# Performance work log

Hardware: AMD Instinct MI355X
Metric: run time of the kernel (lower is better)

## Reference

```python
import jax, jax.numpy as jnp
import numpy as np

SEQ, B, I, H, L = 2048, 32, 1024, 1024, 2


def setup_inputs() -> dict:
    key = jax.random.key(0)
    ks = jax.random.split(key, 6)
    k = 1.0 / np.sqrt(H)
    x = jax.random.normal(ks[0], (SEQ, B, I), dtype=jnp.float32)
    h0 = jnp.zeros((L, B, H), dtype=jnp.float32)
    # layer 0 W_ih is [H, I]; with I == H all layers stack to [L, H, H]
    W_ih = jax.random.uniform(ks[1], (L, H, H), minval=-k, maxval=k, dtype=jnp.float32)
    W_hh = jax.random.uniform(ks[2], (L, H, H), minval=-k, maxval=k, dtype=jnp.float32)
    b_ih = jax.random.uniform(ks[3], (L, H), minval=-k, maxval=k, dtype=jnp.float32)
    b_hh = jax.random.uniform(ks[4], (L, H), minval=-k, maxval=k, dtype=jnp.float32)
    return {"x": x, "h0": h0, "W_ih": W_ih, "W_hh": W_hh, "b_ih": b_ih, "b_hh": b_hh}


def reference(x, h0, W_ih, W_hh, b_ih, b_hh):
    """Stacked tanh RNN, seq-first input [T, B, I]. Returns (h_history [T,B,H], h_T [L,B,H])."""
    num_layers = W_ih.shape[0]

    def step(h_prev, x_t):
        inp = x_t
        hs = []
        for l in range(num_layers):  # small fixed layer count
            a = (jnp.einsum('bd,cd->bc', inp, W_ih[l])
                 + jnp.einsum('bd,cd->bc', h_prev[l], W_hh[l])
                 + b_ih[l] + b_hh[l])
            hl = jnp.tanh(a)
            hs.append(hl)
            inp = hl
        h_new = jnp.stack(hs)  # [L, B, H]
        return h_new, h_new[-1]

    h_T, h_history = jax.lax.scan(step, h0, x)
    return h_history, h_T
```

## Files before the change

### kernel.cpp

```cpp
#include <hip/hip_runtime.h>
#include <stdint.h>

#define T_SEQ 2048
#define NB 32
#define NH 1024
#define HH (NH*NH)
#define HIST_ELEMS ((size_t)T_SEQ*NB*NH)

typedef __attribute__((ext_vector_type(8))) short bf16x8;
typedef __attribute__((ext_vector_type(4))) float f32x4;
typedef __attribute__((ext_vector_type(4))) int   i32x4;
typedef __attribute__((ext_vector_type(2))) int   i32x2;
typedef __attribute__((ext_vector_type(4))) short s16x4;

__device__ __forceinline__ unsigned short bf16rne(float f){
  union { float f; unsigned u; } v; v.f = f;
  unsigned u = v.u;
  return (unsigned short)((u + 0x7FFFu + ((u >> 16) & 1u)) >> 16);
}
__device__ __forceinline__ float bf16tof(unsigned short s){
  union { unsigned u; float f; } v; v.u = ((unsigned)s) << 16; return v.f;
}
__device__ __forceinline__ float fast_tanh(float x){
  float ax = fabsf(x);
  float e  = __expf(-2.0f*ax);
  float t  = (1.0f - e) / (1.0f + e);
  return copysignf(t, x);
}

__device__ __forceinline__ i32x4 ld128_cohere(const void* p){
  i32x4 d;
  asm volatile("global_load_dwordx4 %0, %1, off sc0 sc1" : "=v"(d) : "v"(p) : "memory");
  return d;
}
__device__ __forceinline__ void st64_cohere(void* p, i32x2 v){
  asm volatile("global_store_dwordx2 %0, %1, off sc0 sc1" :: "v"(p), "v"(v) : "memory");
}
__device__ __forceinline__ void st32_cohere(void* p, int v){
  asm volatile("global_store_dword %0, %1, off sc0 sc1" :: "v"(p), "v"(v) : "memory");
}
__device__ __forceinline__ void vmem_drain(){
  asm volatile("s_waitcnt vmcnt(0)" ::: "memory");
  __builtin_amdgcn_sched_barrier(0);
}

__global__ __launch_bounds__(256)
void pre_gemm(const float* __restrict__ x,
              const float* __restrict__ Wih,
              const float* __restrict__ bih,
              const float* __restrict__ bhh,
              _Float16* __restrict__ pre0)
{
  __shared__ float As[128][36];
  const int tid  = threadIdx.x;
  const int lane = tid & 63;
  const int wave = tid >> 6;
  const int l15  = lane & 15;
  const int l4   = lane >> 4;
  const int n0   = blockIdx.x * 128;
  const int m0   = blockIdx.y * 128;
  const int qm   = wave >> 1;
  const int qn   = wave & 1;

  f32x4 acc[4][4];
  #pragma unroll
  for (int i = 0; i < 4; ++i)
    #pragma unroll
    for (int j = 0; j < 4; ++j) acc[i][j] = (f32x4){0.f,0.f,0.f,0.f};

  const int sr = tid >> 1;
  const int sh = tid & 1;
  const float* xrow = x + (size_t)(m0 + sr)*NH + sh*16;

  for (int kb = 0; kb < 32; ++kb){
    __syncthreads();
    {
      const float* src = xrow + kb*32;
      f32x4 v0 = *(const f32x4*)(src + 0);
      f32x4 v1 = *(const f32x4*)(src + 4);
      f32x4 v2 = *(const f32x4*)(src + 8);
      f32x4 v3 = *(const f32x4*)(src + 12);
      float* dst = &As[sr][sh*16];
      *(f32x4*)(dst + 0)  = v0;
      *(f32x4*)(dst + 4)  = v1;
      *(f32x4*)(dst + 8)  = v2;
      *(f32x4*)(dst + 12) = v3;
    }
    __syncthreads();

    bf16x8 ahi[4], alo[4];
    #pragma unroll
    for (int mt = 0; mt < 4; ++mt){
      const float* ap = &As[64*qm + 16*mt + l15][l4*8];
      #pragma unroll
      for (int j = 0; j < 8; ++j){
        float a = ap[j];
        unsigned short hb = bf16rne(a);
        ahi[mt][j] = (short)hb;
        alo[mt][j] = (short)bf16rne(a - bf16tof(hb));
      }
    }
    #pragma unroll
    for (int nf = 0; nf < 4; ++nf){
      const int c = n0 + 64*qn + 16*nf + l15;
      const float* wp = Wih + (size_t)c*NH + kb*32 + l4*8;
      bf16x8 bf;
      #pragma unroll
      for (int j = 0; j < 8; ++j) bf[j] = (short)bf16rne(wp[j]);
      #pragma unroll
      for (int mt = 0; mt < 4; ++mt){
        acc[mt][nf] = __builtin_amdgcn_mfma_f32_16x16x32_bf16(ahi[mt], bf, acc[mt][nf], 0,0,0);
        acc[mt][nf] = __builtin_amdgcn_mfma_f32_16x16x32_bf16(alo[mt], bf, acc[mt][nf], 0,0,0);
      }
    }
  }

  #pragma unroll
  for (int nf = 0; nf < 4; ++nf){
    const int c = n0 + 64*qn + 16*nf + l15;
    const float bv = bih[c] + bhh[c];
    #pragma unroll
    for (int mt = 0; mt < 4; ++mt){
      const int mb = m0 + 64*qm + 16*mt + l4*4;
      #pragma unroll
      for (int j = 0; j < 4; ++j)
        pre0[(size_t)(mb + j)*NH + c] = (_Float16)(acc[mt][nf][j] + bv);
    }
  }
}

__global__ __launch_bounds__(256, 1)
void rnn_seq(const float* __restrict__ h0in,
             const float* __restrict__ Wih,
             const float* __restrict__ Whh,
             const float* __restrict__ bih,
             const float* __restrict__ bhh,
             const _Float16* __restrict__ pre0,
             float* __restrict__ dout,
             char* __restrict__ ws)
{
  const int wg   = blockIdx.x;
  const int tid  = threadIdx.x;
  const int lane = tid & 63;
  const int wave = tid >> 6;
  const int l15  = lane & 15;
  const int l4   = lane >> 4;
  const int c0   = wg * 16;

  int*  flags = (int*)ws;
  char* h0buf = ws + 4096;
  char* h1buf = ws + 4096 + 131072;

  bf16x8 wA[3][8];
  {
    const size_t row = (size_t)(c0 + l15) * NH;
    const float* s0 = Whh + row;
    const float* s1 = Wih + HH + row;
    const float* s2 = Whh + HH + row;
    #pragma unroll
    for (int s = 0; s < 8; ++s){
      const int k = wave*256 + s*32 + l4*8;
      #pragma unroll
      for (int j = 0; j < 8; ++j){
        wA[0][s][j] = (short)bf16rne(s0[k+j]);
        wA[1][s][j] = (short)bf16rne(s1[k+j]);
        wA[2][s][j] = (short)bf16rne(s2[k+j]);
      }
    }
  }

  const int elayer = tid >> 7;
  const int eb     = (tid >> 2) & 31;
  const int ecb    = tid & 3;
  const int ecol   = c0 + ecb*4;

  f32x4 bias1 = {0.f,0.f,0.f,0.f};
  if (elayer == 1){
    #pragma unroll
    for (int j = 0; j < 4; ++j)
      bias1[j] = bih[NH + ecol + j] + bhh[NH + ecol + j];
  }

  {
    const float* hs = h0in + (size_t)elayer*NB*NH + (size_t)eb*NH + ecol;
    i32x2 pk;
    pk[0] = (int)bf16rne(hs[0]) | ((int)bf16rne(hs[1]) << 16);
    pk[1] = (int)bf16rne(hs[2]) | ((int)bf16rne(hs[3]) << 16);
    char* dst = (elayer == 0 ? h0buf : h1buf) + 65536 + eb*2048 + ecol*2;
    st64_cohere(dst, pk);
  }
  vmem_drain();
  __syncthreads();
  if (tid == 0) st32_cohere(flags + wg, 1);

  __shared__ float scr[4][4][16][16];
  long spins = 0;

  for (int p = 0; p <= T_SEQ; ++p){
    const bool doL0 = (p < T_SEQ);
    const bool doL1 = (p >= 1);

    s16x4 praw = {0,0,0,0};
    if (elayer == 0 && doL0)
      praw = *(const s16x4*)(pre0 + (size_t)p*(NB*NH) + (size_t)eb*NH + ecol);

    {
      const int target = 1 + p;
      const int* fp = flags + (l15 << 2);
      for (;;){
        i32x4 f = ld128_cohere(fp);
        vmem_drain();
        int ok = (f[0] >= target) && (f[1] >= target) && (f[2] >= target) && (f[3] >= target);
        if (__all(ok)) break;
        if (++spins > (1L << 22)) break;
        __builtin_amdgcn_s_sleep(2);
      }
    }

    const char* h0rd = h0buf + ((p-1)&1)*65536;
    const char* h1rd = h1buf + ((p-2)&1)*65536;
    i32x4 g0[2][8], g1[2][8];
    #pragma unroll
    for (int bt = 0; bt < 2; ++bt){
      const int b = bt*16 + l15;
      #pragma unroll
      for (int s = 0; s < 8; ++s){
        const int d = wave*256 + s*32 + l4*8;
        g0[bt][s] = ld128_cohere(h0rd + b*2048 + d*2);
      }
    }
    if (doL1){
      #pragma unroll
      for (int bt = 0; bt < 2; ++bt){
        const int b = bt*16 + l15;
        #pragma unroll
        for (int s = 0; s < 8; ++s){
          const int d = wave*256 + s*32 + l4*8;
          g1[bt][s] = ld128_cohere(h1rd + b*2048 + d*2);
        }
      }
    }
    vmem_drain();

    f32x4 acc0[2] = {{0,0,0,0},{0,0,0,0}};
    f32x4 acc1[2] = {{0,0,0,0},{0,0,0,0}};
    #pragma unroll
    for (int bt = 0; bt < 2; ++bt){
      #pragma unroll
      for (int s = 0; s < 8; ++s){
        bf16x8 b0 = __builtin_bit_cast(bf16x8, g0[bt][s]);
        if (doL0)
          acc0[bt] = __builtin_amdgcn_mfma_f32_16x16x32_bf16(wA[0][s], b0, acc0[bt], 0,0,0);
        if (doL1){
          acc1[bt] = __builtin_amdgcn_mfma_f32_16x16x32_bf16(wA[1][s], b0, acc1[bt], 0,0,0);
          bf16x8 b1 = __builtin_bit_cast(bf16x8, g1[bt][s]);
          acc1[bt] = __builtin_amdgcn_mfma_f32_16x16x32_bf16(wA[2][s], b1, acc1[bt], 0,0,0);
        }
      }
    }

    *(f32x4*)&scr[wave][0][l15][l4*4] = acc0[0];
    *(f32x4*)&scr[wave][1][l15][l4*4] = acc0[1];
    *(f32x4*)&scr[wave][2][l15][l4*4] = acc1[0];
    *(f32x4*)&scr[wave][3][l15][l4*4] = acc1[1];
    __syncthreads();

    f32x4 sum = {0,0,0,0};
    {
      const int f = elayer*2 + (eb >> 4);
      #pragma unroll
      for (int w = 0; w < 4; ++w)
        sum += *(const f32x4*)&scr[w][f][eb & 15][ecb*4];
    }

    if (elayer == 0){
      if (doL0){
        union { s16x4 v; _Float16 h[4]; } pu; pu.v = praw;
        float hv[4];
        #pragma unroll
        for (int j = 0; j < 4; ++j)
          hv[j] = fast_tanh(sum[j] + (float)pu.h[j]);
        i32x2 pk;
        pk[0] = (int)bf16rne(hv[0]) | ((int)bf16rne(hv[1]) << 16);
        pk[1] = (int)bf16rne(hv[2]) | ((int)bf16rne(hv[3]) << 16);
        st64_cohere(h0buf + (p&1)*65536 + eb*2048 + ecol*2, pk);
        if (p == T_SEQ-1){
          f32x4 o = {hv[0], hv[1], hv[2], hv[3]};
          *(f32x4*)(dout + HIST_ELEMS + (size_t)eb*NH + ecol) = o;
        }
      }
    } else {
      if (doL1){
        float hv[4];
        #pragma unroll
        for (int j = 0; j < 4; ++j)
          hv[j] = fast_tanh(sum[j] + bias1[j]);
        i32x2 pk;
        pk[0] = (int)bf16rne(hv[0]) | ((int)bf16rne(hv[1]) << 16);
        pk[1] = (int)bf16rne(hv[2]) | ((int)bf16rne(hv[3]) << 16);
        st64_cohere(h1buf + ((p-1)&1)*65536 + eb*2048 + ecol*2, pk);
        f32x4 o = {hv[0], hv[1], hv[2], hv[3]};
        *(f32x4*)(dout + (size_t)(p-1)*(NB*NH) + (size_t)eb*NH + ecol) = o;
        if (p == T_SEQ)
          *(f32x4*)(dout + HIST_ELEMS + (size_t)NB*NH + (size_t)eb*NH + ecol) = o;
      }
    }

    vmem_drain();
    __syncthreads();
    if (tid == 0) st32_cohere(flags + wg, 2 + p);
  }
}

extern "C" void kernel_launch(void* const* d_in, const int* in_sizes, int n_in,
                              void* d_out, int out_size, void* d_ws, size_t ws_size,
                              hipStream_t stream)
{
  (void)in_sizes; (void)n_in; (void)out_size;
  const float* x   = (const float*)d_in[0];
  const float* h0  = (const float*)d_in[1];
  const float* Wih = (const float*)d_in[2];
  const float* Whh = (const float*)d_in[3];
  const float* bih = (const float*)d_in[4];
  const float* bhh = (const float*)d_in[5];
  float* out = (float*)d_out;
  char*  ws  = (char*)d_ws;

  const size_t PRE0_OFF = (size_t)1 << 20;
  const size_t NEED = PRE0_OFF + (size_t)T_SEQ*NB*NH*sizeof(_Float16);
  if (ws_size < NEED) return;

  _Float16* pre0 = (_Float16*)(ws + PRE0_OFF);

  hipMemsetAsync(ws, 0, 4096, stream);
  pre_gemm<<<dim3(8, 512), 256, 0, stream>>>(x, Wih, bih, bhh, pre0);
  rnn_seq<<<dim3(64), 256, 0, stream>>>(h0, Wih, Whh, bih, bhh, pre0, out, ws);
}
```

Baseline: 17.46 ms.

## Confine persistent RNN workgroups to a single XCC team of 32

Measured after the change: 15.42 ms. 1.13x faster.

```diff
diff --git a/kernel.cpp b/kernel.cpp
--- a/kernel.cpp
+++ b/kernel.cpp
@@ -6,6 +6,7 @@
 #define NH 1024
 #define HH (NH*NH)
 #define HIST_ELEMS ((size_t)T_SEQ*NB*NH)
+#define TEAM 32
 
 typedef __attribute__((ext_vector_type(8))) short bf16x8;
 typedef __attribute__((ext_vector_type(4))) float f32x4;
@@ -28,16 +29,23 @@
   return copysignf(t, x);
 }
 
-__device__ __forceinline__ i32x4 ld128_cohere(const void* p){
+__device__ __forceinline__ i32x4 ld128_c(const void* p){
   i32x4 d;
   asm volatile("global_load_dwordx4 %0, %1, off sc0 sc1" : "=v"(d) : "v"(p) : "memory");
   return d;
 }
-__device__ __forceinline__ void st64_cohere(void* p, i32x2 v){
+__device__ __forceinline__ void st64_c(void* p, i32x2 v){
   asm volatile("global_store_dwordx2 %0, %1, off sc0 sc1" :: "v"(p), "v"(v) : "memory");
 }
-__device__ __forceinline__ void st32_cohere(void* p, int v){
+__device__ __forceinline__ void st32_c(void* p, unsigned v){
   asm volatile("global_store_dword %0, %1, off sc0 sc1" :: "v"(p), "v"(v) : "memory");
+}
+__device__ __forceinline__ unsigned ld32_c(const void* p){
+  unsigned d;
+  asm volatile("global_load_dword %0, %1, off sc0 sc1\n\ts_waitcnt vmcnt(0)"
+               : "=v"(d) : "v"(p) : "memory");
+  __builtin_amdgcn_sched_barrier(0);
+  return d;
 }
 __device__ __forceinline__ void vmem_drain(){
   asm volatile("s_waitcnt vmcnt(0)" ::: "memory");
@@ -139,21 +147,72 @@
              float* __restrict__ dout,
              char* __restrict__ ws)
 {
-  const int wg   = blockIdx.x;
   const int tid  = threadIdx.x;
   const int lane = tid & 63;
   const int wave = tid >> 6;
   const int l15  = lane & 15;
   const int l4   = lane >> 4;
-  const int c0   = wg * 16;
-
-  int*  flags = (int*)ws;
-  char* h0buf = ws + 4096;
-  char* h1buf = ws + 4096 + 131072;
-
-  bf16x8 wA[3][8];
-  {
-    const size_t row = (size_t)(c0 + l15) * NH;
+
+  unsigned* counts = (unsigned*)ws;
+  unsigned* winner = (unsigned*)(ws + 64);
+  unsigned* bcast  = (unsigned*)(ws + 128);
+  unsigned* flags  = (unsigned*)(ws + 4096);
+  char* h0buf = ws + 8192;
+  char* h1buf = ws + 8192 + 131072;
+
+  __shared__ unsigned sh_go, sh_rank, sh_base;
+
+  if (tid == 0){
+    unsigned xcc;
+    asm volatile("s_getreg_b32 %0, hwreg(HW_REG_XCC_ID)" : "=s"(xcc));
+    xcc &= 7u;
+    unsigned slot = atomicAdd(&counts[xcc], 1u);
+    unsigned go = 0, rank = 0, base = 0;
+    if (slot < TEAM){
+      if (slot == TEAM - 1) atomicCAS(winner, 0u, xcc + 1u);
+      unsigned w = 0; long c = 0;
+      for (;;){
+        w = ld32_c(winner);
+        if (w) break;
+        if (++c > (1L << 20)) break;
+        __builtin_amdgcn_s_sleep(8);
+      }
+      if (w == xcc + 1u){ go = 1; rank = slot; }
+    }
+    if (go){
+      if (rank == 0){
+        unsigned mx = 0;
+        for (int i = 0; i < TEAM; ++i){ unsigned v = ld32_c(flags + i); if (v > mx) mx = v; }
+        if (mx > 0xF0000000u) mx = 0;
+        for (int i = 0; i < TEAM; ++i) st32_c(flags + i, mx);
+        st32_c(bcast + 0, mx);
+        vmem_drain();
+        st32_c(bcast + 1, 1u);
+        vmem_drain();
+        base = mx;
+      } else {
+        long c = 0;
+        for (;;){
+          unsigned r = ld32_c(bcast + 1);
+          if (r) break;
+          if (++c > (1L << 23)) break;
+          __builtin_amdgcn_s_sleep(2);
+        }
+        base = ld32_c(bcast + 0);
+      }
+    }
+    sh_go = go; sh_rank = rank; sh_base = base;
+  }
+  __syncthreads();
+  if (!sh_go) return;
+  const unsigned rank = sh_rank;
+  const unsigned base = sh_base;
+  const int c0 = (int)rank * 32;
+
+  bf16x8 wA[3][2][8];
+  #pragma unroll
+  for (int cf = 0; cf < 2; ++cf){
+    const size_t row = (size_t)(c0 + cf*16 + l15) * NH;
     const float* s0 = Whh + row;
     const float* s1 = Wih + HH + row;
     const float* s2 = Whh + HH + row;
@@ -162,38 +221,38 @@
       const int k = wave*256 + s*32 + l4*8;
       #pragma unroll
       for (int j = 0; j < 8; ++j){
-        wA[0][s][j] = (short)bf16rne(s0[k+j]);
-        wA[1][s][j] = (short)bf16rne(s1[k+j]);
-        wA[2][s][j] = (short)bf16rne(s2[k+j]);
-      }
-    }
-  }
-
-  const int elayer = tid >> 7;
-  const int eb     = (tid >> 2) & 31;
-  const int ecb    = tid & 3;
-  const int ecol   = c0 + ecb*4;
-
-  f32x4 bias1 = {0.f,0.f,0.f,0.f};
-  if (elayer == 1){
-    #pragma unroll
-    for (int j = 0; j < 4; ++j)
-      bias1[j] = bih[NH + ecol + j] + bhh[NH + ecol + j];
-  }
+        wA[0][cf][s][j] = (short)bf16rne(s0[k+j]);
+        wA[1][cf][s][j] = (short)bf16rne(s1[k+j]);
+        wA[2][cf][s][j] = (short)bf16rne(s2[k+j]);
+      }
+    }
+  }
+
+  const int eb   = tid >> 3;
+  const int ecb  = tid & 7;
+  const int ecol = c0 + ecb*4;
+
+  f32x4 bias1;
+  #pragma unroll
+  for (int j = 0; j < 4; ++j)
+    bias1[j] = bih[NH + ecol + j] + bhh[NH + ecol + j];
 
   {
-    const float* hs = h0in + (size_t)elayer*NB*NH + (size_t)eb*NH + ecol;
-    i32x2 pk;
-    pk[0] = (int)bf16rne(hs[0]) | ((int)bf16rne(hs[1]) << 16);
-    pk[1] = (int)bf16rne(hs[2]) | ((int)bf16rne(hs[3]) << 16);
-    char* dst = (elayer == 0 ? h0buf : h1buf) + 65536 + eb*2048 + ecol*2;
-    st64_cohere(dst, pk);
+    const float* hs0 = h0in + (size_t)eb*NH + ecol;
+    const float* hs1 = h0in + (size_t)NB*NH + (size_t)eb*NH + ecol;
+    i32x2 p0, p1;
+    p0[0] = (int)bf16rne(hs0[0]) | ((int)bf16rne(hs0[1]) << 16);
+    p0[1] = (int)bf16rne(hs0[2]) | ((int)bf16rne(hs0[3]) << 16);
+    p1[0] = (int)bf16rne(hs1[0]) | ((int)bf16rne(hs1[1]) << 16);
+    p1[1] = (int)bf16rne(hs1[2]) | ((int)bf16rne(hs1[3]) << 16);
+    st64_c(h0buf + 65536 + eb*2048 + ecol*2, p0);
+    st64_c(h1buf + 65536 + eb*2048 + ecol*2, p1);
   }
   vmem_drain();
   __syncthreads();
-  if (tid == 0) st32_cohere(flags + wg, 1);
-
-  __shared__ float scr[4][4][16][16];
+  if (tid == 0) st32_c(flags + rank, base + 1u);
+
+  __shared__ float scr[4][8][16][20];
   long spins = 0;
 
   for (int p = 0; p <= T_SEQ; ++p){
@@ -201,21 +260,23 @@
     const bool doL1 = (p >= 1);
 
     s16x4 praw = {0,0,0,0};
-    if (elayer == 0 && doL0)
+    if (doL0)
       praw = *(const s16x4*)(pre0 + (size_t)p*(NB*NH) + (size_t)eb*NH + ecol);
 
-    {
-      const int target = 1 + p;
-      const int* fp = flags + (l15 << 2);
+    if (wave == 0){
+      const unsigned target = base + 1u + (unsigned)p;
+      const unsigned* fp = flags + ((lane & 7) << 2);
       for (;;){
-        i32x4 f = ld128_cohere(fp);
+        i32x4 f = ld128_c(fp);
         vmem_drain();
-        int ok = (f[0] >= target) && (f[1] >= target) && (f[2] >= target) && (f[3] >= target);
+        int ok = ((unsigned)f[0] >= target) && ((unsigned)f[1] >= target)
+              && ((unsigned)f[2] >= target) && ((unsigned)f[3] >= target);
         if (__all(ok)) break;
-        if (++spins > (1L << 22)) break;
-        __builtin_amdgcn_s_sleep(2);
-      }
-    }
+        if (++spins > (1L << 25)) break;
+        __builtin_amdgcn_s_sleep(1);
+      }
+    }
+    __syncthreads();
 
     const char* h0rd = h0buf + ((p-1)&1)*65536;
     const char* h1rd = h1buf + ((p-2)&1)*65536;
@@ -226,7 +287,7 @@
       #pragma unroll
       for (int s = 0; s < 8; ++s){
         const int d = wave*256 + s*32 + l4*8;
-        g0[bt][s] = ld128_cohere(h0rd + b*2048 + d*2);
+        g0[bt][s] = ld128_c(h0rd + b*2048 + d*2);
       }
     }
     if (doL1){
@@ -236,79 +297,85 @@
         #pragma unroll
         for (int s = 0; s < 8; ++s){
           const int d = wave*256 + s*32 + l4*8;
-          g1[bt][s] = ld128_cohere(h1rd + b*2048 + d*2);
+          g1[bt][s] = ld128_c(h1rd + b*2048 + d*2);
         }
       }
     }
     vmem_drain();
 
-    f32x4 acc0[2] = {{0,0,0,0},{0,0,0,0}};
-    f32x4 acc1[2] = {{0,0,0,0},{0,0,0,0}};
-    #pragma unroll
-    for (int bt = 0; bt < 2; ++bt){
-      #pragma unroll
-      for (int s = 0; s < 8; ++s){
-        bf16x8 b0 = __builtin_bit_cast(bf16x8, g0[bt][s]);
-        if (doL0)
-          acc0[bt] = __builtin_amdgcn_mfma_f32_16x16x32_bf16(wA[0][s], b0, acc0[bt], 0,0,0);
-        if (doL1){
-          acc1[bt] = __builtin_amdgcn_mfma_f32_16x16x32_bf16(wA[1][s], b0, acc1[bt], 0,0,0);
-          bf16x8 b1 = __builtin_bit_cast(bf16x8, g1[bt][s]);
-          acc1[bt] = __builtin_amdgcn_mfma_f32_16x16x32_bf16(wA[2][s], b1, acc1[bt], 0,0,0);
+    f32x4 acc0[2][2] = {{{0,0,0,0},{0,0,0,0}},{{0,0,0,0},{0,0,0,0}}};
+    f32x4 acc1[2][2] = {{{0,0,0,0},{0,0,0,0}},{{0,0,0,0},{0,0,0,0}}};
+    #pragma unroll
+    for (int cf = 0; cf < 2; ++cf){
+      #pragma unroll
+      for (int bt = 0; bt < 2; ++bt){
+        #pragma unroll
+        for (int s = 0; s < 8; ++s){
+          bf16x8 b0 = __builtin_bit_cast(bf16x8, g0[bt][s]);
+          if (doL0)
+            acc0[cf][bt] = __builtin_amdgcn_mfma_f32_16x16x32_bf16(wA[0][cf][s], b0, acc0[cf][bt], 0,0,0);
+          if (doL1){
+            acc1[cf][bt] = __builtin_amdgcn_mfma_f32_16x16x32_bf16(wA[1][cf][s], b0, acc1[cf][bt], 0,0,0);
+            bf16x8 b1 = __builtin_bit_cast(bf16x8, g1[bt][s]);
+            acc1[cf][bt] = __builtin_amdgcn_mfma_f32_16x16x32_bf16(wA[2][cf][s], b1, acc1[cf][bt], 0,0,0);
+          }
         }
       }
     }
 
-    *(f32x4*)&scr[wave][0][l15][l4*4] = acc0[0];
-    *(f32x4*)&scr[wave][1][l15][l4*4] = acc0[1];
-    *(f32x4*)&scr[wave][2][l15][l4*4] = acc1[0];
-    *(f32x4*)&scr[wave][3][l15][l4*4] = acc1[1];
+    #pragma unroll
+    for (int cf = 0; cf < 2; ++cf){
+      #pragma unroll
+      for (int bt = 0; bt < 2; ++bt){
+        *(f32x4*)&scr[wave][(cf<<1)|bt][l15][l4*4]     = acc0[cf][bt];
+        *(f32x4*)&scr[wave][4|(cf<<1)|bt][l15][l4*4]   = acc1[cf][bt];
+      }
+    }
     __syncthreads();
 
-    f32x4 sum = {0,0,0,0};
-    {
-      const int f = elayer*2 + (eb >> 4);
-      #pragma unroll
-      for (int w = 0; w < 4; ++w)
-        sum += *(const f32x4*)&scr[w][f][eb & 15][ecb*4];
-    }
-
-    if (elayer == 0){
-      if (doL0){
-        union { s16x4 v; _Float16 h[4]; } pu; pu.v = praw;
-        float hv[4];
-        #pragma unroll
-        for (int j = 0; j < 4; ++j)
-          hv[j] = fast_tanh(sum[j] + (float)pu.h[j]);
-        i32x2 pk;
-        pk[0] = (int)bf16rne(hv[0]) | ((int)bf16rne(hv[1]) << 16);
-        pk[1] = (int)bf16rne(hv[2]) | ((int)bf16rne(hv[3]) << 16);
-        st64_cohere(h0buf + (p&1)*65536 + eb*2048 + ecol*2, pk);
-        if (p == T_SEQ-1){
-          f32x4 o = {hv[0], hv[1], hv[2], hv[3]};
-          *(f32x4*)(dout + HIST_ELEMS + (size_t)eb*NH + ecol) = o;
-        }
-      }
-    } else {
-      if (doL1){
-        float hv[4];
-        #pragma unroll
-        for (int j = 0; j < 4; ++j)
-          hv[j] = fast_tanh(sum[j] + bias1[j]);
-        i32x2 pk;
-        pk[0] = (int)bf16rne(hv[0]) | ((int)bf16rne(hv[1]) << 16);
-        pk[1] = (int)bf16rne(hv[2]) | ((int)bf16rne(hv[3]) << 16);
-        st64_cohere(h1buf + ((p-1)&1)*65536 + eb*2048 + ecol*2, pk);
-        f32x4 o = {hv[0], hv[1], hv[2], hv[3]};
-        *(f32x4*)(dout + (size_t)(p-1)*(NB*NH) + (size_t)eb*NH + ecol) = o;
-        if (p == T_SEQ)
-          *(f32x4*)(dout + HIST_ELEMS + (size_t)NB*NH + (size_t)eb*NH + ecol) = o;
-      }
+    const int fL0 = ((ecb >> 2) << 1) | (eb >> 4);
+    f32x4 s0v = {0,0,0,0}, s1v = {0,0,0,0};
+    #pragma unroll
+    for (int w = 0; w < 4; ++w){
+      s0v += *(const f32x4*)&scr[w][fL0][eb & 15][(ecb & 3)*4];
+      s1v += *(const f32x4*)&scr[w][4|fL0][eb & 15][(ecb & 3)*4];
+    }
+
+    float hv0[4], hv1[4];
+    if (doL0){
+      union { s16x4 v; _Float16 h[4]; } pu; pu.v = praw;
+      #pragma unroll
+      for (int j = 0; j < 4; ++j)
+        hv0[j] = fast_tanh(s0v[j] + (float)pu.h[j]);
+      i32x2 pk;
+      pk[0] = (int)bf16rne(hv0[0]) | ((int)bf16rne(hv0[1]) << 16);
+      pk[1] = (int)bf16rne(hv0[2]) | ((int)bf16rne(hv0[3]) << 16);
+      st64_c(h0buf + (p&1)*65536 + eb*2048 + ecol*2, pk);
+    }
+    if (doL1){
+      #pragma unroll
+      for (int j = 0; j < 4; ++j)
+        hv1[j] = fast_tanh(s1v[j] + bias1[j]);
+      i32x2 pk;
+      pk[0] = (int)bf16rne(hv1[0]) | ((int)bf16rne(hv1[1]) << 16);
+      pk[1] = (int)bf16rne(hv1[2]) | ((int)bf16rne(hv1[3]) << 16);
+      st64_c(h1buf + ((p-1)&1)*65536 + eb*2048 + ecol*2, pk);
     }
 
     vmem_drain();
     __syncthreads();
-    if (tid == 0) st32_cohere(flags + wg, 2 + p);
+    if (tid == 0) st32_c(flags + rank, base + 2u + (unsigned)p);
+
+    if (doL1){
+      f32x4 o = {hv1[0], hv1[1], hv1[2], hv1[3]};
+      *(f32x4*)(dout + (size_t)(p-1)*(NB*NH) + (size_t)eb*NH + ecol) = o;
+      if (p == T_SEQ)
+        *(f32x4*)(dout + HIST_ELEMS + (size_t)NB*NH + (size_t)eb*NH + ecol) = o;
+    }
+    if (doL0 && p == T_SEQ-1){
+      f32x4 o = {hv0[0], hv0[1], hv0[2], hv0[3]};
+      *(f32x4*)(dout + HIST_ELEMS + (size_t)eb*NH + ecol) = o;
+    }
   }
 }
 
@@ -332,7 +399,7 @@
 
   _Float16* pre0 = (_Float16*)(ws + PRE0_OFF);
 
-  hipMemsetAsync(ws, 0, 4096, stream);
+  hipMemsetAsync(ws, 0, 256, stream);
   pre_gemm<<<dim3(8, 512), 256, 0, stream>>>(x, Wih, bih, bhh, pre0);
-  rnn_seq<<<dim3(64), 256, 0, stream>>>(h0, Wih, Whh, bih, bhh, pre0, out, ws);
-}
+  rnn_seq<<<dim3(512), 256, 0, stream>>>(h0, Wih, Whh, bih, bhh, pre0, out, ws);
+}
```
